# Optimization experiments

Hardware: AMD Instinct MI355X
Metric: run time of the kernel (lower is better)

The kernel has to match this reference:

```python
import jax, jax.numpy as jnp
import numpy as np

B, S, T, E, H, Vt, Vs, M = 16, 64, 64, 256, 512, 32000, 32000, 100
J = 2 * M + 1


def _lstm(x, lengths, Wx, Wh, b, reverse=False):
    # TF LSTMCell (forget_bias=1.0) with sequence_length masking, optional reverse_sequence.
    Bn, Tn, _ = x.shape
    Hn = Wh.shape[0]
    tpos = jnp.arange(Tn)
    ridx = None
    if reverse:
        ridx = jnp.where(tpos[None, :] < lengths[:, None], lengths[:, None] - 1 - tpos[None, :], tpos[None, :])
        x = jnp.take_along_axis(x, ridx[:, :, None], axis=1)
    mask = (tpos[:, None] < lengths[None, :])[:, :, None]  # [T,B,1]
    xT = jnp.swapaxes(x, 0, 1)  # [T,B,E]

    def step(carry, inp):
        h, c = carry
        xt, mt = inp
        g = xt @ Wx + h @ Wh + b
        i, j, f, o = jnp.split(g, 4, axis=-1)
        c_new = jax.nn.sigmoid(f + 1.0) * c + jax.nn.sigmoid(i) * jnp.tanh(j)
        h_new = jax.nn.sigmoid(o) * jnp.tanh(c_new)
        c2 = jnp.where(mt, c_new, c)
        h2 = jnp.where(mt, h_new, h)
        return (h2, c2), jnp.where(mt, h_new, jnp.zeros_like(h_new))

    init = (jnp.zeros((Bn, Hn), x.dtype), jnp.zeros((Bn, Hn), x.dtype))
    _, ys = jax.lax.scan(step, init, (xT, mask))
    ys = jnp.swapaxes(ys, 0, 1)  # [B,T,H]
    if reverse:
        ys = jnp.take_along_axis(ys, ridx[:, :, None], axis=1)
    return ys


def setup_inputs() -> dict:
    key = jax.random.key(0)
    ks = jax.random.split(key, 24)
    sc = 0.05
    n = lambda k, shape: (jax.random.normal(k, shape, jnp.float32) * sc)
    inp = {
        "sources": jax.random.randint(ks[0], (B, S), 0, Vs, jnp.int32),
        "targets": jax.random.randint(ks[1], (B, T), 0, Vt, jnp.int32),
        "targets_null": jnp.array([Vt - 1], jnp.int32),
        "target_lengths": jax.random.randint(ks[2], (B,), T // 2, T + 1, jnp.int32),
        "emb": n(ks[3], (Vt, E)),
        "nnW": n(ks[4], (E, H)),
        "nnb": jnp.zeros((H,), jnp.float32),
        "Wx_fw": n(ks[5], (E, 4 * H)),
        "Wh_fw": n(ks[6], (H, 4 * H)),
        "b_fw": jnp.zeros((4 * H,), jnp.float32),
        "Wx_bw": n(ks[7], (E, 4 * H)),
        "Wh_bw": n(ks[8], (H, 4 * H)),
        "b_bw": jnp.zeros((4 * H,), jnp.float32),
        "Wproj_e": n(ks[9], (2 * H, H)),
        "Wv": n(ks[10], (H, Vs)),
        "bv": jnp.zeros((Vs,), jnp.float32),
        "Wproj_t": n(ks[11], (2 * H, E)),
        "Wj": n(ks[12], (H, J)),
        "bj": jnp.zeros((J,), jnp.float32),
        "Wp0": n(ks[13], (H, 1)),
        "bp0": jnp.zeros((1,), jnp.float32),
    }
    return inp


def reference(sources, targets, targets_null, target_lengths, emb, nnW, nnb,
              Wx_fw, Wh_fw, b_fw, Wx_bw, Wh_bw, b_bw, Wproj_e, Wv, bv,
              Wproj_t, Wj, bj, Wp0, bp0):
    x = emb[targets]                              # [B,T,E]
    x_null = emb[targets_null]                    # [1,E]
    null_state = jnp.tanh(x_null @ nnW + nnb)     # [1,H]
    h_fw = _lstm(x, target_lengths, Wx_fw, Wh_fw, b_fw, False)
    h_bw = _lstm(x, target_lengths, Wx_bw, Wh_bw, b_bw, True)
    h_cat = jnp.concatenate([h_fw, h_bw], axis=-1)  # [B,T,2H]

    # ---- emission ----
    ts = h_cat @ Wproj_e                          # [B,T,H]
    probs = jax.nn.softmax(ts @ Wv + bv, axis=-1)             # [B,T,Vs]
    null_probs = jax.nn.softmax(null_state @ Wv + bv, axis=-1)  # [1,Vs]
    e_word = jnp.take_along_axis(probs, sources[:, None, :].astype(jnp.int32), axis=2)  # [B,T,S]
    e_null = jnp.broadcast_to(null_probs[0][sources][:, None, :], e_word.shape)
    emission = jnp.concatenate([e_word, e_null], axis=1)       # [B,2T,S]

    # ---- transition ----
    tt = jnp.tanh((h_cat @ Wproj_t) @ nnW + nnb)  # [B,T,H]
    jump = jax.nn.softmax(tt @ Wj + bj, axis=-1)  # [B,T,J]
    p0 = jax.nn.sigmoid(tt @ Wp0 + bp0)[..., 0]   # [B,T]
    Tn = targets.shape[1]
    # entry (i,j) <- jump[i, M + j - i] (the tf.map_fn gather over word_idx)
    idx = M + jnp.arange(Tn)[None, :] - jnp.arange(Tn)[:, None]  # [T,T]
    jw = jnp.take_along_axis(jump, jnp.broadcast_to(idx[None], (jump.shape[0], Tn, Tn)), axis=2)  # [B,T,T]
    eye = jnp.eye(Tn, dtype=jw.dtype)
    half = jnp.concatenate([jw, p0[:, :, None] * eye], axis=2)            # [B,T,2T]
    transition = jnp.concatenate([half, half], axis=1)                    # [B,2T,2T]
    lhalf = jnp.concatenate([jnp.log(jw), jnp.log(p0)[:, :, None] * eye], axis=2)
    transition_log = jnp.concatenate([lhalf, lhalf], axis=1)
    return emission, transition, transition_log
```

## Files before the change

kernel.cpp:

```cpp
#include <hip/hip_runtime.h>
#include <hip/hip_bf16.h>
#include <math.h>

#define Bn 16
#define Sn 64
#define Tn 64
#define En 256
#define Hn 512
#define VS 32000
#define Jn 201
#define Mn 100

#define O_HCATF  0
#define O_DENOM  524288
#define O_NULLD  525312
#define O_SLOTS  525376
#define O_HBUF   527424
#define ZERO_N   560192
#define O_NS     560192
#define O_TS     560704
#define O_TSF    1084992
#define O_TTPRE  1347136
#define O_TTPF   1609280
#define O_TT     1740352
#define O_XF     2264640
#define O_WXFW   2395712
#define O_WXBW   2657856
#define O_WPEF   2920000
#define O_WPTF   3182144
#define O_NNWF   3313216
#define O_GX     3378752

typedef __attribute__((ext_vector_type(8))) short short8;
typedef __attribute__((ext_vector_type(4))) float f32x4;

__device__ __forceinline__ float sigf(float x) { return 1.0f / (1.0f + expf(-x)); }
__device__ __forceinline__ unsigned short tobf(float x) {
    __hip_bfloat16 h = __float2bfloat16(x);
    return *reinterpret_cast<unsigned short*>(&h);
}

__device__ __forceinline__ void dconvA(const float* __restrict__ A, uint4* __restrict__ out,
                                       int K, const int* __restrict__ gidx, int g) {
    int Kd = K >> 5;
    int lane = g & 63, t = g >> 6;
    int ks = t % Kd, mt = t / Kd;
    int m = mt * 16 + (lane & 15);
    int k0 = ks * 32 + (lane >> 4) * 8;
    const float* p = (gidx ? A + (size_t)gidx[m] * K : A + (size_t)m * K) + k0;
    float4 f0 = *(const float4*)(p);
    float4 f1 = *(const float4*)(p + 4);
    unsigned short u[8] = {tobf(f0.x), tobf(f0.y), tobf(f0.z), tobf(f0.w),
                           tobf(f1.x), tobf(f1.y), tobf(f1.z), tobf(f1.w)};
    out[g] = *(uint4*)u;
}

__device__ __forceinline__ void dconvB(const float* __restrict__ B, uint4* __restrict__ out,
                                       int N, int K, int g) {
    int Kd = K >> 5;
    int lane = g & 63, t = g >> 6;
    int ks = t % Kd, nt = t / Kd;
    int n = nt * 16 + (lane & 15);
    int k0 = ks * 32 + (lane >> 4) * 8;
    const float* p = B + (size_t)k0 * N + n;
    unsigned short u[8];
#pragma unroll
    for (int j = 0; j < 8; j++) u[j] = tobf(p[(size_t)j * N]);
    out[g] = *(uint4*)u;
}

__global__ __launch_bounds__(256) void convA2_k(const float* __restrict__ ttpre,
                                                uint4* __restrict__ ttpf,
                                                const float* __restrict__ ts,
                                                uint4* __restrict__ tsf) {
    int blk = blockIdx.x, tid = threadIdx.x;
    if (blk < 128) dconvA(ttpre, ttpf, 256, nullptr, blk * 256 + tid);
    else           dconvA(ts, tsf, 512, nullptr, (blk - 128) * 256 + tid);
}

__global__ __launch_bounds__(256) void mega_prep_k(float4* __restrict__ zdst, int zn4,
                                                   const float* __restrict__ emb,
                                                   const int* __restrict__ targets,
                                                   uint4* __restrict__ xf,
                                                   const float* __restrict__ wxfw, uint4* __restrict__ wxfwf,
                                                   const float* __restrict__ wxbw, uint4* __restrict__ wxbwf,
                                                   const float* __restrict__ wpe, uint4* __restrict__ wpef,
                                                   const float* __restrict__ wpt, uint4* __restrict__ wptf,
                                                   const float* __restrict__ nnw, uint4* __restrict__ nnwf) {
    int blk = blockIdx.x, tid = threadIdx.x;
    if (blk < 548) {
        int i = blk * 256 + tid;
        if (i < zn4) zdst[i] = make_float4(0.f, 0.f, 0.f, 0.f);
    } else if (blk < 676) {
        dconvA(emb, xf, 256, targets, (blk - 548) * 256 + tid);
    } else if (blk < 932) {
        dconvB(wxfw, wxfwf, 2048, 256, (blk - 676) * 256 + tid);
    } else if (blk < 1188) {
        dconvB(wxbw, wxbwf, 2048, 256, (blk - 932) * 256 + tid);
    } else if (blk < 1444) {
        dconvB(wpe, wpef, 512, 1024, (blk - 1188) * 256 + tid);
    } else if (blk < 1572) {
        dconvB(wpt, wptf, 256, 1024, (blk - 1444) * 256 + tid);
    } else {
        dconvB(nnw, nnwf, 512, 256, (blk - 1572) * 256 + tid);
    }
}

template <int ACT>
__device__ __forceinline__ void gemm_body(const uint4* __restrict__ af,
                                          const uint4* __restrict__ bf,
                                          const float* __restrict__ bias,
                                          float* __restrict__ C, int N, int Kd,
                                          int bx, int by) {
    int tid = threadIdx.x, w = tid >> 6, lane = tid & 63;
    int ntb = bx * 8 + w * 2;
    int mtb = by * 8;
    f32x4 acc[8][2];
#pragma unroll
    for (int i = 0; i < 8; i++)
#pragma unroll
        for (int j = 0; j < 2; j++) acc[i][j] = 0.0f;
    for (int ks = 0; ks < Kd; ++ks) {
        uint4 b0 = bf[(size_t)(ntb * Kd + ks) * 64 + lane];
        uint4 b1 = bf[(size_t)((ntb + 1) * Kd + ks) * 64 + lane];
#pragma unroll
        for (int i = 0; i < 8; i++) {
            uint4 a = af[(size_t)((mtb + i) * Kd + ks) * 64 + lane];
            acc[i][0] = __builtin_amdgcn_mfma_f32_16x16x32_bf16(
                *reinterpret_cast<short8*>(&a), *reinterpret_cast<short8*>(&b0), acc[i][0], 0, 0, 0);
            acc[i][1] = __builtin_amdgcn_mfma_f32_16x16x32_bf16(
                *reinterpret_cast<short8*>(&a), *reinterpret_cast<short8*>(&b1), acc[i][1], 0, 0, 0);
        }
    }
    int n0 = ntb * 16 + (lane & 15);
    int q = lane >> 4;
    float bs0 = bias ? bias[n0] : 0.f;
    float bs1 = bias ? bias[n0 + 16] : 0.f;
#pragma unroll
    for (int i = 0; i < 8; i++)
#pragma unroll
        for (int r = 0; r < 4; r++) {
            int m = (mtb + i) * 16 + q * 4 + r;
            float v0 = acc[i][0][r] + bs0;
            float v1 = acc[i][1][r] + bs1;
            if (ACT == 1) { v0 = tanhf(v0); v1 = tanhf(v1); }
            C[(size_t)m * N + n0] = v0;
            C[(size_t)m * N + n0 + 16] = v1;
        }
}

template <int ACT>
__global__ __launch_bounds__(256) void gemm_mfma_k(const uint4* __restrict__ af,
                                                   const uint4* __restrict__ bf,
                                                   const float* __restrict__ bias,
                                                   float* __restrict__ C, int N, int Kd) {
    gemm_body<ACT>(af, bf, bias, C, N, Kd, blockIdx.x, blockIdx.y);
}

__global__ __launch_bounds__(256) void gx_gemm_k(const uint4* __restrict__ xf,
                                                 const uint4* __restrict__ wxfwf,
                                                 const uint4* __restrict__ wxbwf,
                                                 const float* __restrict__ b_fw,
                                                 const float* __restrict__ b_bw,
                                                 float* __restrict__ gx) {
    int bx = blockIdx.x;
    if (bx < 16) gemm_body<0>(xf, wxfwf, b_fw, gx, 2048, 8, bx, blockIdx.y);
    else         gemm_body<0>(xf, wxbwf, b_bw, gx + 2097152, 2048, 8, bx - 16, blockIdx.y);
}

__global__ __launch_bounds__(256) void proj_gemm_k(const uint4* __restrict__ hcatf,
                                                   const uint4* __restrict__ wpef,
                                                   const uint4* __restrict__ wptf,
                                                   float* __restrict__ ts,
                                                   float* __restrict__ ttpre) {
    int bx = blockIdx.x;
    if (bx < 4) gemm_body<0>(hcatf, wpef, nullptr, ts, 512, 32, bx, blockIdx.y);
    else        gemm_body<0>(hcatf, wptf, nullptr, ttpre, 256, 32, bx - 4, blockIdx.y);
}

__global__ __launch_bounds__(256, 1) void lstm_fused_k(const float* __restrict__ wh_fw,
                                                       const float* __restrict__ wh_bw,
                                                       const float* __restrict__ gx,
                                                       const int* __restrict__ lengths,
                                                       unsigned* __restrict__ hbuf32,
                                                       unsigned* __restrict__ hcat32,
                                                       unsigned* __restrict__ slots,
                                                       const float* __restrict__ Wv,
                                                       const float* __restrict__ emb,
                                                       const int* __restrict__ tnull,
                                                       const float* __restrict__ nnW,
                                                       const float* __restrict__ nnb,
                                                       const float* __restrict__ bv,
                                                       float* __restrict__ ns,
                                                       float* __restrict__ nd) {
    int blk = blockIdx.x;
    int tid = threadIdx.x;

    if (blk >= 32) {
        __shared__ float xn[En];
        __shared__ float nsl[Hn];
        __shared__ float red[4];
        int bid = blk - 32;
        xn[tid] = emb[(size_t)tnull[0] * En + tid];
        __syncthreads();
#pragma unroll
        for (int hh = 0; hh < 2; hh++) {
            int h = tid + hh * 256;
            float a = nnb[h];
            for (int e = 0; e < En; e++) a += xn[e] * nnW[(size_t)e * Hn + h];
            float v = tanhf(a);
            nsl[h] = v;
            if (bid == 0) ns[h] = v;
        }
        __syncthreads();
        int v = bid * 256 + tid;
        float a = bv[v];
        for (int k = 0; k < Hn; k++) a += nsl[k] * Wv[(size_t)k * VS + v];
        float e = expf(a);
        for (int o = 1; o < 64; o <<= 1) e += __shfl_xor(e, o);
        if ((tid & 63) == 0) red[tid >> 6] = e;
        __syncthreads();
        if (tid == 0) atomicAdd(nd, red[0] + red[1] + red[2] + red[3]);
        return;
    }

    __shared__ uint4 whf[8192];
    __shared__ float raw[32][129];
    __shared__ int lenS[16];
    int dir = blk >> 4;
    int u0 = (blk & 15) * 32;
    const float* wh = dir ? wh_bw : wh_fw;
    if (tid < 16) lenS[tid] = lengths[tid];

    for (int chunk = 0; chunk < 16; ++chunk) {
#pragma unroll
        for (int it = 0; it < 16; ++it) {
            int li = it * 256 + tid;
            int kl = li >> 7, c = li & 127;
            int g = c >> 5, ub = c & 31;
            raw[kl][c] = wh[(size_t)(chunk * 32 + kl) * 2048 + g * 512 + u0 + ub];
        }
        __syncthreads();
#pragma unroll
        for (int it = 0; it < 2; ++it) {
            int idx = tid * 2 + it;
            int w = idx >> 7, t = (idx >> 6) & 1, lane = idx & 63;
            int n = lane & 15, uu = n >> 1, p = n & 1;
            int cc = (t * 2 + p) * 32 + w * 8 + uu;
            int kb = (lane >> 4) * 8;
            unsigned short u8[8];
#pragma unroll
            for (int j = 0; j < 8; j++) u8[j] = tobf(raw[kb + j][cc]);
            whf[((w * 2 + t) * 16 + chunk) * 64 + lane] = *(uint4*)u8;
        }
        __syncthreads();
    }

    int wv = tid >> 6, lane = tid & 63;
    int n = lane & 15, uu = n >> 1, q = lane >> 4;
    int u = u0 + wv * 8 + uu;
    float creg[4] = {0.f, 0.f, 0.f, 0.f};
    unsigned short hbf[4] = {0, 0, 0, 0};

    for (int s = 0; s < 64; ++s) {
        float gxi[4], gxj[4], gxf[4], gxo[4];
#pragma unroll
        for (int r = 0; r < 4; r++) {
            int b = q * 4 + r;
            int len = lenS[b];
            int tc = dir ? (len - 1 - s) : s;
            tc = tc < 0 ? 0 : tc;
            const float* gp = gx + (size_t)dir * 2097152 + (size_t)(b * 64 + tc) * 2048 + u;
            gxi[r] = gp[0]; gxj[r] = gp[512]; gxf[r] = gp[1024]; gxo[r] = gp[1536];
        }
        const unsigned long long* hb64 =
            (const unsigned long long*)(hbuf32 + (((s & 1) * 2 + dir) * 16) * 256);
        unsigned long long h64[32];
#pragma unroll
        for (int ks = 0; ks < 16; ks++) {
            int idx = n * 128 + ks * 8 + q * 2;
            h64[2 * ks] = __hip_atomic_load(hb64 + idx, __ATOMIC_RELAXED, __HIP_MEMORY_SCOPE_AGENT);
            h64[2 * ks + 1] = __hip_atomic_load(hb64 + idx + 1, __ATOMIC_RELAXED, __HIP_MEMORY_SCOPE_AGENT);
        }
        f32x4 acc0 = {0.f, 0.f, 0.f, 0.f}, acc1 = {0.f, 0.f, 0.f, 0.f};
#pragma unroll
        for (int ks = 0; ks < 16; ks++) {
            unsigned long long av[2] = {h64[2 * ks], h64[2 * ks + 1]};
            short8 a = *reinterpret_cast<short8*>(av);
            uint4 b0 = whf[((wv * 2 + 0) * 16 + ks) * 64 + lane];
            uint4 b1 = whf[((wv * 2 + 1) * 16 + ks) * 64 + lane];
            acc0 = __builtin_amdgcn_mfma_f32_16x16x32_bf16(a, *reinterpret_cast<short8*>(&b0), acc0, 0, 0, 0);
            acc1 = __builtin_amdgcn_mfma_f32_16x16x32_bf16(a, *reinterpret_cast<short8*>(&b1), acc1, 0, 0, 0);
        }
#pragma unroll
        for (int r = 0; r < 4; r++) {
            float jvv = __shfl_xor(acc0[r], 1);
            float ovv = __shfl_xor(acc1[r], 1);
            int b = q * 4 + r;
            int len = lenS[b];
            float gi = acc0[r] + gxi[r];
            float gj = jvv + gxj[r];
            float gf = acc1[r] + gxf[r];
            float go = ovv + gxo[r];
            float cn = sigf(gf + 1.0f) * creg[r] + sigf(gi) * tanhf(gj);
            float hn = sigf(go) * tanhf(cn);
            if (s < len) { creg[r] = cn; hbf[r] = tobf(hn); }
        }
#pragma unroll
        for (int r = 0; r < 4; r++) {
            unsigned self = hbf[r];
            unsigned part = (unsigned)__shfl_xor((int)self, 2) & 0xffffu;
            if ((n & 3) == 0) {
                unsigned pk = self | (part << 16);
                int b = q * 4 + r;
                __hip_atomic_store(
                    hbuf32 + ((((s + 1) & 1) * 2 + dir) * 16 + b) * 256 + (u >> 1), pk,
                    __ATOMIC_RELAXED, __HIP_MEMORY_SCOPE_AGENT);
                int len = lenS[b];
                if (s < len) {
                    int tin = dir ? (len - 1 - s) : s;
                    int row = b * 64 + tin, col = dir * 512 + u;
                    int mt = row >> 4, ksx = col >> 5;
                    int lanep = (row & 15) | (((col >> 3) & 3) << 4);
                    hcat32[(size_t)(((mt * 32 + ksx) * 64 + lanep) * 4) + ((col & 7) >> 1)] = pk;
                }
            }
        }
        if (s == 63) break;
        __syncthreads();
        if (tid == 0)
            __hip_atomic_store(&slots[blk * 64], (unsigned)(s + 1), __ATOMIC_RELAXED,
                               __HIP_MEMORY_SCOPE_AGENT);
        if (tid < 16) {
            while (__hip_atomic_load(&slots[(dir * 16 + tid) * 64], __ATOMIC_RELAXED,
                                     __HIP_MEMORY_SCOPE_AGENT) < (unsigned)(s + 1)) {
                __builtin_amdgcn_s_sleep(1);
            }
        }
        __syncthreads();
    }
}

__global__ __launch_bounds__(256) void phaseA_mfma_k(const uint4* __restrict__ tsb,
                                                     const float* __restrict__ Wv,
                                                     const float* __restrict__ bv,
                                                     float* __restrict__ denom) {
    __shared__ uint4 wls[8192];
    __shared__ float redL[4][128];
    int tid = threadIdx.x;
    int wave = tid >> 6, lane = tid & 63;
    for (int it = 0; it < 32; ++it) {
        int g = it * 256 + tid;
        int gl = g & 63, t = g >> 6;
        int ks = t & 15, tl = t >> 4;
        int nt = blockIdx.x * 8 + tl;
        int nn = nt * 16 + (gl & 15);
        int k0 = ks * 32 + (gl >> 4) * 8;
        const float* p = Wv + (size_t)k0 * VS + nn;
        unsigned short u[8];
#pragma unroll
        for (int j = 0; j < 8; j++) u[j] = tobf(p[(size_t)j * VS]);
        wls[g] = *(uint4*)u;
    }
    __syncthreads();

    int ntbase = blockIdx.x * 8 + wave * 2;
    float bv0 = bv[ntbase * 16 + (lane & 15)];
    float bv1 = bv[(ntbase + 1) * 16 + (lane & 15)];
    int q = lane >> 4;
    for (int mc = 0; mc < 8; ++mc) {
        f32x4 acc[8][2];
#pragma unroll
        for (int i = 0; i < 8; i++)
#pragma unroll
            for (int j = 0; j < 2; j++) acc[i][j] = 0.0f;
#pragma unroll 4
        for (int ks = 0; ks < 16; ++ks) {
            short8 a[8], b[2];
#pragma unroll
            for (int i = 0; i < 8; i++) {
                int mt = mc * 8 + i;
                uint4 t = tsb[(size_t)(mt * 16 + ks) * 64 + lane];
                a[i] = *reinterpret_cast<short8*>(&t);
            }
#pragma unroll
            for (int j = 0; j < 2; j++) {
                uint4 t = wls[((wave * 2 + j) * 16 + ks) * 64 + lane];
                b[j] = *reinterpret_cast<short8*>(&t);
            }
#pragma unroll
            for (int i = 0; i < 8; i++)
#pragma unroll
                for (int j = 0; j < 2; j++)
                    acc[i][j] = __builtin_amdgcn_mfma_f32_16x16x32_bf16(a[i], b[j], acc[i][j], 0, 0, 0);
        }
#pragma unroll
        for (int i = 0; i < 8; i++) {
#pragma unroll
            for (int r = 0; r < 4; r++) {
                float e = __expf(acc[i][0][r] + bv0) + __expf(acc[i][1][r] + bv1);
                e += __shfl_xor(e, 1);
                e += __shfl_xor(e, 2);
                e += __shfl_xor(e, 4);
                e += __shfl_xor(e, 8);
                if ((lane & 15) == 0) redL[wave][i * 16 + q * 4 + r] = e;
            }
        }
        __syncthreads();
        if (tid < 128) {
            float v = redL[0][tid] + redL[1][tid] + redL[2][tid] + redL[3][tid];
            atomicAdd(&denom[mc * 128 + tid], v);
        }
        __syncthreads();
    }
}

__global__ __launch_bounds__(512) void emission_k(const float* __restrict__ ts,
                                                  const float* __restrict__ Wv,
                                                  const float* __restrict__ bv,
                                                  const int* __restrict__ sources,
                                                  const float* __restrict__ ns,
                                                  const float* __restrict__ denom,
                                                  const float* __restrict__ nulld,
                                                  float* __restrict__ em) {
    __shared__ float colv[512];
    __shared__ float red[64][9];
    __shared__ float red2[8];
    __shared__ float env_s, bvc_s;
    int b = blockIdx.y, sc = blockIdx.x;
    int tid = threadIdx.x;
    for (int qq = 0; qq < 8; ++qq) {
        int s = sc * 8 + qq;
        int c = sources[b * 64 + s];
        __syncthreads();
        colv[tid] = Wv[(size_t)tid * VS + c];
        if (tid == 0) bvc_s = bv[c];
        __syncthreads();
        int r = tid & 63, ksl = tid >> 6;
        const float* tr = ts + (size_t)(b * 64 + r) * 512 + ksl * 64;
        float p = 0.f;
#pragma unroll
        for (int k4 = 0; k4 < 16; k4++) {
            float4 t4 = *(const float4*)(tr + k4 * 4);
            float4 c4 = *(const float4*)&colv[ksl * 64 + k4 * 4];
            p += t4.x * c4.x + t4.y * c4.y + t4.z * c4.z + t4.w * c4.w;
        }
        red[r][ksl] = p;
        if (tid < 8) {
            float pn = 0.f;
#pragma unroll
            for (int k4 = 0; k4 < 16; k4++) {
                float4 n4 = *(const float4*)(ns + tid * 64 + k4 * 4);
                float4 c4 = *(const float4*)&colv[tid * 64 + k4 * 4];
                pn += n4.x * c4.x + n4.y * c4.y + n4.z * c4.z + n4.w * c4.w;
            }
            red2[tid] = pn;
        }
        __syncthreads();
        if (tid < 64) {
            float dot = red[tid][0] + red[tid][1] + red[tid][2] + red[tid][3] +
                        red[tid][4] + red[tid][5] + red[tid][6] + red[tid][7];
            float ew = expf(dot + bvc_s) / denom[b * 64 + tid];
            em[(size_t)(b * 128 + tid) * 64 + s] = ew;
        } else if (tid == 64) {
            float dn = red2[0] + red2[1] + red2[2] + red2[3] +
                       red2[4] + red2[5] + red2[6] + red2[7];
            env_s = expf(dn + bvc_s) / nulld[0];
        }
        __syncthreads();
        if (tid < 64) em[(size_t)(b * 128 + 64 + tid) * 64 + s] = env_s;
    }
}

__global__ __launch_bounds__(256) void transition_k(const float* __restrict__ tt,
                                                    const float* __restrict__ Wj,
                                                    const float* __restrict__ bj,
                                                    const float* __restrict__ Wp0,
                                                    const float* __restrict__ bp0,
                                                    float* __restrict__ trans,
                                                    float* __restrict__ tlog) {
    __shared__ float ttl[512];
    __shared__ float jrow[Jn], ljrow[Jn];
    __shared__ float sred[256];
    __shared__ float p0_s, lp0_s;
    int blk = blockIdx.x;
    int b = blk >> 6, i = blk & 63;
    int tid = threadIdx.x;
    {
        const float* trr = tt + (size_t)blk * 512;
        if (tid < 128) *(float4*)&ttl[tid * 4] = *(const float4*)(trr + tid * 4);
    }
    __syncthreads();
    bool isj = tid < Jn;
    bool isp = tid == Jn;
    float l = 0.f;
    if (isj || isp) {
        const float* wb = isj ? (Wj + tid) : Wp0;
        int stride = isj ? Jn : 1;
        float a = isj ? bj[tid] : bp0[0];
        for (int k = 0; k < 512; k++) a += ttl[k] * wb[(size_t)k * stride];
        l = a;
    }
    sred[tid] = isj ? l : -1e30f;
    __syncthreads();
    for (int o = 128; o > 0; o >>= 1) {
        if (tid < o) sred[tid] = fmaxf(sred[tid], sred[tid + o]);
        __syncthreads();
    }
    float m = sred[0];
    __syncthreads();
    float ex = isj ? expf(l - m) : 0.f;
    sred[tid] = ex;
    __syncthreads();
    for (int o = 128; o > 0; o >>= 1) {
        if (tid < o) sred[tid] += sred[tid + o];
        __syncthreads();
    }
    float S = sred[0];
    if (isj) {
        jrow[tid] = ex / S;
        ljrow[tid] = (l - m) - logf(S);
    }
    if (isp) {
        float pv = 1.f / (1.f + expf(-l));
        p0_s = pv;
        lp0_s = logf(pv);
    }
    __syncthreads();
    if (tid < 128) {
        int j = tid;
        float tv, lv;
        if (j < 64) {
            int id = Mn + j - i;
            tv = jrow[id];
            lv = ljrow[id];
        } else {
            bool dg = (j - 64) == i;
            tv = dg ? p0_s : 0.f;
            lv = dg ? lp0_s : 0.f;
        }
        size_t r1 = (size_t)(b * 128 + i) * 128 + j;
        size_t r2 = (size_t)(b * 128 + 64 + i) * 128 + j;
        trans[r1] = tv;
        trans[r2] = tv;
        tlog[r1] = lv;
        tlog[r2] = lv;
    }
}

extern "C" void kernel_launch(void* const* d_in, const int* in_sizes, int n_in,
                              void* d_out, int out_size, void* d_ws, size_t ws_size,
                              hipStream_t stream) {
    const int* sources = (const int*)d_in[0];
    const int* targets = (const int*)d_in[1];
    const int* tnull = (const int*)d_in[2];
    const int* lengths = (const int*)d_in[3];
    const float* emb = (const float*)d_in[4];
    const float* nnW = (const float*)d_in[5];
    const float* nnb = (const float*)d_in[6];
    const float* Wx_fw = (const float*)d_in[7];
    const float* Wh_fw = (const float*)d_in[8];
    const float* b_fw = (const float*)d_in[9];
    const float* Wx_bw = (const float*)d_in[10];
    const float* Wh_bw = (const float*)d_in[11];
    const float* b_bw = (const float*)d_in[12];
    const float* Wproj_e = (const float*)d_in[13];
    const float* Wv = (const float*)d_in[14];
    const float* bv = (const float*)d_in[15];
    const float* Wproj_t = (const float*)d_in[16];
    const float* Wj = (const float*)d_in[17];
    const float* bj = (const float*)d_in[18];
    const float* Wp0 = (const float*)d_in[19];
    const float* bp0 = (const float*)d_in[20];

    float* ws = (float*)d_ws;
    float* out = (float*)d_out;
    float* out_em = out;
    float* out_tr = out + 131072;
    float* out_tl = out + 131072 + 262144;

    mega_prep_k<<<1636, 256, 0, stream>>>((float4*)ws, ZERO_N / 4,
                                          emb, targets, (uint4*)(ws + O_XF),
                                          Wx_fw, (uint4*)(ws + O_WXFW),
                                          Wx_bw, (uint4*)(ws + O_WXBW),
                                          Wproj_e, (uint4*)(ws + O_WPEF),
                                          Wproj_t, (uint4*)(ws + O_WPTF),
                                          nnW, (uint4*)(ws + O_NNWF));

    gx_gemm_k<<<dim3(32, 8), 256, 0, stream>>>((uint4*)(ws + O_XF), (uint4*)(ws + O_WXFW),
                                               (uint4*)(ws + O_WXBW), b_fw, b_bw, ws + O_GX);

    lstm_fused_k<<<157, 256, 0, stream>>>(Wh_fw, Wh_bw, ws + O_GX, lengths,
                                          (unsigned*)(ws + O_HBUF), (unsigned*)(ws + O_HCATF),
                                          (unsigned*)(ws + O_SLOTS),
                                          Wv, emb, tnull, nnW, nnb, bv,
                                          ws + O_NS, ws + O_NULLD);

    proj_gemm_k<<<dim3(6, 8), 256, 0, stream>>>((uint4*)(ws + O_HCATF), (uint4*)(ws + O_WPEF),
                                                (uint4*)(ws + O_WPTF), ws + O_TS, ws + O_TTPRE);

    convA2_k<<<384, 256, 0, stream>>>(ws + O_TTPRE, (uint4*)(ws + O_TTPF),
                                      ws + O_TS, (uint4*)(ws + O_TSF));
    gemm_mfma_k<1><<<dim3(4, 8), 256, 0, stream>>>((uint4*)(ws + O_TTPF), (uint4*)(ws + O_NNWF),
                                                   nnb, ws + O_TT, 512, 8);

    phaseA_mfma_k<<<250, 256, 0, stream>>>((const uint4*)(ws + O_TSF),
                                           Wv, bv, ws + O_DENOM);

    emission_k<<<dim3(8, 16), 512, 0, stream>>>(ws + O_TS, Wv, bv, sources, ws + O_NS,
                                                ws + O_DENOM, ws + O_NULLD, out_em);

    transition_k<<<1024, 256, 0, stream>>>(ws + O_TT, Wj, bj, Wp0, bp0, out_tr, out_tl);
}
```

Baseline: 877.0 us.

## Overlap weight conversions and Wv column gather with LSTM kernel idle blocks

Moves the bf16 conversions of Wproj_e, Wproj_t and nnW out of the prep kernel and into extra blocks of the LSTM kernel, so they run alongside the latency-bound recurrence. Those extra blocks also pre-gather the Wv columns indexed by the source tokens into a compact buffer. The emission kernel then reads that buffer contiguously instead of doing strided column reads from the large Wv matrix. The gather buffer reuses the XF region, which is safe only if XF is dead after gx_gemm. The extra blocks could also compete with the persistent LSTM blocks for CUs or bandwidth.

```diff
diff --git a/kernel.cpp b/kernel.cpp
--- a/kernel.cpp
+++ b/kernel.cpp
@@ -24,6 +24,7 @@
 #define O_TTPF   1609280
 #define O_TT     1740352
 #define O_XF     2264640
+#define O_WVC    2264640
 #define O_WXFW   2395712
 #define O_WXBW   2657856
 #define O_WPEF   2920000
@@ -83,10 +84,7 @@
                                                    const int* __restrict__ targets,
                                                    uint4* __restrict__ xf,
                                                    const float* __restrict__ wxfw, uint4* __restrict__ wxfwf,
-                                                   const float* __restrict__ wxbw, uint4* __restrict__ wxbwf,
-                                                   const float* __restrict__ wpe, uint4* __restrict__ wpef,
-                                                   const float* __restrict__ wpt, uint4* __restrict__ wptf,
-                                                   const float* __restrict__ nnw, uint4* __restrict__ nnwf) {
+                                                   const float* __restrict__ wxbw, uint4* __restrict__ wxbwf) {
     int blk = blockIdx.x, tid = threadIdx.x;
     if (blk < 548) {
         int i = blk * 256 + tid;
@@ -95,14 +93,8 @@
         dconvA(emb, xf, 256, targets, (blk - 548) * 256 + tid);
     } else if (blk < 932) {
         dconvB(wxfw, wxfwf, 2048, 256, (blk - 676) * 256 + tid);
-    } else if (blk < 1188) {
+    } else {
         dconvB(wxbw, wxbwf, 2048, 256, (blk - 932) * 256 + tid);
-    } else if (blk < 1444) {
-        dconvB(wpe, wpef, 512, 1024, (blk - 1188) * 256 + tid);
-    } else if (blk < 1572) {
-        dconvB(wpt, wptf, 256, 1024, (blk - 1444) * 256 + tid);
-    } else {
-        dconvB(nnw, nnwf, 512, 256, (blk - 1572) * 256 + tid);
     }
 }
 
@@ -192,10 +184,40 @@
                                                        const float* __restrict__ nnb,
                                                        const float* __restrict__ bv,
                                                        float* __restrict__ ns,
-                                                       float* __restrict__ nd) {
+                                                       float* __restrict__ nd,
+                                                       const int* __restrict__ sources,
+                                                       float* __restrict__ wvc,
+                                                       const float* __restrict__ wpe, uint4* __restrict__ wpef,
+                                                       const float* __restrict__ wpt, uint4* __restrict__ wptf,
+                                                       const float* __restrict__ nnw2, uint4* __restrict__ nnwf) {
     int blk = blockIdx.x;
     int tid = threadIdx.x;
 
+    if (blk >= 669) {
+        dconvB(nnw2, nnwf, 512, 256, (blk - 669) * 256 + tid);
+        return;
+    }
+    if (blk >= 541) {
+        dconvB(wpt, wptf, 256, 1024, (blk - 541) * 256 + tid);
+        return;
+    }
+    if (blk >= 285) {
+        dconvB(wpe, wpef, 512, 1024, (blk - 285) * 256 + tid);
+        return;
+    }
+    if (blk >= 157) {
+        int cb = blk - 157;
+#pragma unroll
+        for (int cc = 0; cc < 8; ++cc) {
+            int ci = cb * 8 + cc;
+            int c = sources[ci];
+            float v0 = Wv[(size_t)tid * VS + c];
+            float v1 = Wv[(size_t)(tid + 256) * VS + c];
+            wvc[(size_t)ci * 512 + tid] = v0;
+            wvc[(size_t)ci * 512 + 256 + tid] = v1;
+        }
+        return;
+    }
     if (blk >= 32) {
         __shared__ float xn[En];
         __shared__ float nsl[Hn];
@@ -416,7 +438,7 @@
 }
 
 __global__ __launch_bounds__(512) void emission_k(const float* __restrict__ ts,
-                                                  const float* __restrict__ Wv,
+                                                  const float* __restrict__ wvc,
                                                   const float* __restrict__ bv,
                                                   const int* __restrict__ sources,
                                                   const float* __restrict__ ns,
@@ -431,10 +453,10 @@
     int tid = threadIdx.x;
     for (int qq = 0; qq < 8; ++qq) {
         int s = sc * 8 + qq;
-        int c = sources[b * 64 + s];
-        __syncthreads();
-        colv[tid] = Wv[(size_t)tid * VS + c];
-        if (tid == 0) bvc_s = bv[c];
+        int ci = b * 64 + s;
+        __syncthreads();
+        colv[tid] = wvc[(size_t)ci * 512 + tid];
+        if (tid == 0) bvc_s = bv[sources[ci]];
         __syncthreads();
         int r = tid & 63, ksl = tid >> 6;
         const float* tr = ts + (size_t)(b * 64 + r) * 512 + ksl * 64;
@@ -579,22 +601,23 @@
     float* out_tr = out + 131072;
     float* out_tl = out + 131072 + 262144;
 
-    mega_prep_k<<<1636, 256, 0, stream>>>((float4*)ws, ZERO_N / 4,
+    mega_prep_k<<<1188, 256, 0, stream>>>((float4*)ws, ZERO_N / 4,
                                           emb, targets, (uint4*)(ws + O_XF),
                                           Wx_fw, (uint4*)(ws + O_WXFW),
-                                          Wx_bw, (uint4*)(ws + O_WXBW),
+                                          Wx_bw, (uint4*)(ws + O_WXBW));
+
+    gx_gemm_k<<<dim3(32, 8), 256, 0, stream>>>((uint4*)(ws + O_XF), (uint4*)(ws + O_WXFW),
+                                               (uint4*)(ws + O_WXBW), b_fw, b_bw, ws + O_GX);
+
+    lstm_fused_k<<<733, 256, 0, stream>>>(Wh_fw, Wh_bw, ws + O_GX, lengths,
+                                          (unsigned*)(ws + O_HBUF), (unsigned*)(ws + O_HCATF),
+                                          (unsigned*)(ws + O_SLOTS),
+                                          Wv, emb, tnull, nnW, nnb, bv,
+                                          ws + O_NS, ws + O_NULLD,
+                                          sources, ws + O_WVC,
                                           Wproj_e, (uint4*)(ws + O_WPEF),
                                           Wproj_t, (uint4*)(ws + O_WPTF),
                                           nnW, (uint4*)(ws + O_NNWF));
-
-    gx_gemm_k<<<dim3(32, 8), 256, 0, stream>>>((uint4*)(ws + O_XF), (uint4*)(ws + O_WXFW),
-                                               (uint4*)(ws + O_WXBW), b_fw, b_bw, ws + O_GX);
-
-    lstm_fused_k<<<157, 256, 0, stream>>>(Wh_fw, Wh_bw, ws + O_GX, lengths,
-                                          (unsigned*)(ws + O_HBUF), (unsigned*)(ws + O_HCATF),
-                                          (unsigned*)(ws + O_SLOTS),
-                                          Wv, emb, tnull, nnW, nnb, bv,
-                                          ws + O_NS, ws + O_NULLD);
 
     proj_gemm_k<<<dim3(6, 8), 256, 0, stream>>>((uint4*)(ws + O_HCATF), (uint4*)(ws + O_WPEF),
                                                 (uint4*)(ws + O_WPTF), ws + O_TS, ws + O_TTPRE);
@@ -607,7 +630,7 @@
     phaseA_mfma_k<<<250, 256, 0, stream>>>((const uint4*)(ws + O_TSF),
                                            Wv, bv, ws + O_DENOM);
 
-    emission_k<<<dim3(8, 16), 512, 0, stream>>>(ws + O_TS, Wv, bv, sources, ws + O_NS,
+    emission_k<<<dim3(8, 16), 512, 0, stream>>>(ws + O_TS, ws + O_WVC, bv, sources, ws + O_NS,
                                                 ws + O_DENOM, ws + O_NULLD, out_em);
 
     transition_k<<<1024, 256, 0, stream>>>(ws + O_TT, Wj, bj, Wp0, bp0, out_tr, out_tl);
```

Result: no change. 872.3 us (-0.5%).
